# Kernel optimization log

Hardware: AMD Instinct MI355X
Metric: run time of the kernel (lower is better)

## Reference

```python
import jax, jax.numpy as jnp
import numpy as np

B, N, E = 2, 50000, 400000
C_IN, D, C, S, H, L, FFN = 5, 2, 128, 32, 8, 4, 512
COORD_F, TIME_F, FREQ_BASE, BETA = 8, 4, 1000.0, 1.0
HD = C // H


def setup_inputs() -> dict:
    key = jax.random.key(0)
    ks = jax.random.split(key, 32)
    sc = 0.02
    inp = {
        'inputs': jax.random.normal(ks[0], (B, N, C_IN), jnp.float32),
        'coords': jax.random.uniform(ks[1], (B, N, D), jnp.float32),
        't_norm': jax.random.uniform(ks[2], (B,), jnp.float32),
        'adj_indices': jax.random.randint(ks[3], (2, E), 0, N, jnp.int64 if jax.config.jax_enable_x64 else jnp.int32),
        'adj_values': jax.random.uniform(ks[4], (E,), jnp.float32) * 0.25,  # ~1/avg_degree for stable magnitudes
        'freq_matrix': jax.random.normal(ks[5], (D, COORD_F), jnp.float32),
        'embed_W': jax.random.normal(ks[6], (C_IN + 2 * COORD_F + 2 * TIME_F, C), jnp.float32) * sc,
        'embed_b': jnp.zeros((C,), jnp.float32),
        'ln1_g': jnp.ones((L, C), jnp.float32),
        'ln1_b': jnp.zeros((L, C), jnp.float32),
        'Wslice': jax.random.normal(ks[7], (L, C, S), jnp.float32) * sc,
        'bslice': jnp.zeros((L, S), jnp.float32),
        'Wfront': jax.random.normal(ks[8], (L, C, S), jnp.float32) * sc,
        'bfront': jnp.zeros((L, S), jnp.float32),
        'Win': jax.random.normal(ks[9], (L, C, 3 * C), jnp.float32) * sc,
        'b_in': jnp.zeros((L, 3 * C), jnp.float32),
        'Wout': jax.random.normal(ks[10], (L, C, C), jnp.float32) * sc,
        'bout': jnp.zeros((L, C), jnp.float32),
        'ln2_g': jnp.ones((L, C), jnp.float32),
        'ln2_b': jnp.zeros((L, C), jnp.float32),
        'Wff1': jax.random.normal(ks[11], (L, C, FFN), jnp.float32) * sc,
        'bff1': jnp.zeros((L, FFN), jnp.float32),
        'Wff2': jax.random.normal(ks[12], (L, FFN, C), jnp.float32) * sc,
        'bff2': jnp.zeros((L, C), jnp.float32),
        'proj_W': jax.random.normal(ks[13], (C, C_IN), jnp.float32) * sc,
        'proj_b': jnp.zeros((C_IN,), jnp.float32),
    }
    return inp


def _layer_norm(x, g, b, eps=1e-5):
    m = jnp.mean(x, -1, keepdims=True)
    v = jnp.mean(jnp.square(x - m), -1, keepdims=True)
    return (x - m) * jax.lax.rsqrt(v + eps) * g + b


def _forward(inputs, coords, t_norm, adj_indices, adj_values, freq_matrix,
             embed_W, embed_b, ln1_g, ln1_b, Wslice, bslice, Wfront, bfront,
             Win, b_in, Wout, bout, ln2_g, ln2_b, Wff1, bff1, Wff2, bff2,
             proj_W, proj_b):
    rows, cols = adj_indices[0], adj_indices[1]
    b, n = coords.shape[0], coords.shape[1]
    # spatial Fourier encoding (B,N,2*COORD_F)
    p = 2.0 * jnp.pi * (coords @ freq_matrix)
    sp_enc = jnp.concatenate([jnp.sin(p), jnp.cos(p)], -1)
    # temporal encoding (B,N,2*TIME_F)
    omega = FREQ_BASE ** (-jnp.arange(TIME_F, dtype=jnp.float32) / TIME_F)
    ang = omega[None, :] * (t_norm * FREQ_BASE)[:, None]
    t_enc = jnp.broadcast_to(jnp.concatenate([jnp.sin(ang), jnp.cos(ang)], -1)[:, None, :], (b, n, 2 * TIME_F))
    x = jnp.concatenate([inputs, sp_enc, t_enc], -1) @ embed_W + embed_b  # (B,N,C)
    weights_all = []
    for l in range(L):
        h = _layer_norm(x, ln1_g[l], ln1_b[l])
        # sparse adjacency aggregation: y[r] += a_e * h[c] (duplicates sum == coalesce)
        contrib = adj_values[None, :, None] * h[:, cols, :]  # (B,E,C)
        h_local = jax.vmap(lambda cb: jax.ops.segment_sum(cb, rows, num_segments=n))(contrib)
        h_front = h - h_local
        logits = h @ Wslice[l] + bslice[l] + BETA * (h_front @ Wfront[l] + bfront[l])
        w = jax.nn.softmax(logits, -1)  # (B,N,S)
        wsum = jnp.maximum(jnp.sum(w, axis=1)[:, :, None], 1e-8)  # (B,S,1)
        slices = jnp.einsum('bns,bnc->bsc', w, h) / wsum  # (B,S,C)
        # slice-space MHA (self-attention on S tokens)
        qkv = slices @ Win[l] + b_in[l]
        q, k, v = jnp.split(qkv, 3, axis=-1)
        def split_heads(t):
            return t.reshape(b, S, H, HD).transpose(0, 2, 1, 3)  # (B,H,S,HD)
        qh, kh, vh = split_heads(q), split_heads(k), split_heads(v)
        attn = jax.nn.softmax(jnp.einsum('bhqd,bhkd->bhqk', qh, kh) / jnp.sqrt(jnp.float32(HD)), -1)
        o = jnp.einsum('bhqk,bhkd->bhqd', attn, vh).transpose(0, 2, 1, 3).reshape(b, S, C)
        slices_out = o @ Wout[l] + bout[l]
        x = x + jnp.einsum('bns,bsc->bnc', w, slices_out)
        h2 = _layer_norm(x, ln2_g[l], ln2_b[l])
        x = x + jax.nn.gelu(h2 @ Wff1[l] + bff1[l], approximate=False) @ Wff2[l] + bff2[l]
        weights_all.append(w)
    out = x @ proj_W + proj_b  # (B,N,C_OUT)
    return out, jnp.stack(weights_all)  # (L,B,N,S)


def reference(inputs, coords, t_norm, adj_indices, adj_values, freq_matrix,
              embed_W, embed_b, ln1_g, ln1_b, Wslice, bslice, Wfront, bfront,
              Win, b_in, Wout, bout, ln2_g, ln2_b, Wff1, bff1, Wff2, bff2,
              proj_W, proj_b):
    return _forward(inputs, coords, t_norm, adj_indices, adj_values, freq_matrix,
                    embed_W, embed_b, ln1_g, ln1_b, Wslice, bslice, Wfront, bfront,
                    Win, b_in, Wout, bout, ln2_g, ln2_b, Wff1, bff1, Wff2, bff2,
                    proj_W, proj_b)
```

## Files before the change

kernel.cpp:

```cpp
#include <hip/hip_runtime.h>
#include <math.h>

#define BATCH 2
#define NN 50000
#define NE 400000
#define C_IN 5
#define CC 128
#define SS 32
#define NH 8
#define NL 4
#define FFN 512
#define COORD_F 8
#define TIME_F 4
#define HD 16
#define BETA 1.0f
#define TWO_PI 6.283185307179586476925287f

#define NTOT (BATCH * NN)
#define FF_MT 128
#define FF_BLOCKS ((NTOT + FF_MT - 1) / FF_MT)
#define MPAD (FF_BLOCKS * FF_MT)
#define NBLK ((NN + 127) / 128)
#define LP_PAD 136
#define H2S 136
#define HIDS 72
#define NREP 16
#define EMB_NPB 8
#define PROJ_NPB 12

typedef unsigned short u16;
typedef unsigned int u32;
typedef __attribute__((ext_vector_type(8))) __bf16 bf16x8;
typedef __attribute__((ext_vector_type(4))) float f32x4;

__device__ __forceinline__ u16 f2bf(float f) {
    union { __bf16 b; u16 u; } v;
    v.b = (__bf16)f;
    return v.u;
}

__device__ __forceinline__ float bf2f(u16 h) {
    union { u32 u; float f; } v; v.u = ((u32)h) << 16;
    return v.f;
}

__device__ __forceinline__ float bf_lo(u32 u) {
    union { u32 u; float f; } v; v.u = u << 16;
    return v.f;
}

__device__ __forceinline__ float bf_hi(u32 u) {
    union { u32 u; float f; } v; v.u = u & 0xffff0000u;
    return v.f;
}

__device__ __forceinline__ float gelu_f(float a) {
    float xx = a * 0.7071067811865475f;
    float ax = fabsf(xx);
    float t = 1.0f / fmaf(0.3275911f, ax, 1.0f);
    float poly = t * fmaf(t, fmaf(t, fmaf(t, fmaf(t, 1.061405429f, -1.453152027f),
                                          1.421413741f), -0.284496736f), 0.254829592f);
    float e = __expf(-ax * ax);
    float erfv = copysignf(fmaf(-poly, e, 1.0f), xx);
    return 0.5f * a * (1.0f + erfv);
}

__global__ void count_deg(const int* rows, int* deg) {
    int e = blockIdx.x * blockDim.x + threadIdx.x;
    if (e < NE) atomicAdd(&deg[rows[e]], 1);
}

__global__ __launch_bounds__(512) void scan_deg(const int* deg, int* rowptr) {
    __shared__ int part[512];
    int t = threadIdx.x;
    const int CH = (NN + 511) / 512;
    int begin = t * CH, end = min(begin + CH, NN);
    int s = 0;
    for (int i = begin; i < end; i++) s += deg[i];
    part[t] = s;
    __syncthreads();
    for (int off = 1; off < 512; off <<= 1) {
        int v = (t >= off) ? part[t - off] : 0;
        __syncthreads();
        part[t] += v;
        __syncthreads();
    }
    int base = (t == 0) ? 0 : part[t - 1];
    for (int i = begin; i < end; i++) { rowptr[i] = base; base += deg[i]; }
    if (t == 511) rowptr[NN] = part[511];
}

__global__ void fill_csr(const int* rows, const int* cols, const float* vals,
                         int* cursor, int* csr_col, float* csr_val) {
    int e = blockIdx.x * blockDim.x + threadIdx.x;
    if (e < NE) {
        int p = atomicAdd(&cursor[rows[e]], 1);
        csr_col[p] = cols[e];
        csr_val[p] = vals[e];
    }
}

__global__ __launch_bounds__(128) void embed_ln1_kernel(const float* __restrict__ inputs,
                                                        const float* __restrict__ coords,
                                                        const float* __restrict__ t_norm,
                                                        const float* __restrict__ freq,
                                                        const float* __restrict__ W,
                                                        const float* __restrict__ bias,
                                                        const float* __restrict__ g,
                                                        const float* __restrict__ bb,
                                                        float* __restrict__ x,
                                                        u16* __restrict__ hbf) {
    int t = threadIdx.x;
    int n0 = blockIdx.x * EMB_NPB;
    __shared__ float feat[EMB_NPB][32];
    __shared__ float sm[EMB_NPB][4];
    if (t < EMB_NPB) {
        int node = n0 + t;
        if (node < NTOT) {
            int b = node / NN;
            float c0 = coords[node * 2 + 0], c1 = coords[node * 2 + 1];
            #pragma unroll
            for (int j = 0; j < 8; j++) {
                float p = TWO_PI * (c0 * freq[j] + c1 * freq[8 + j]);
                feat[t][5 + j] = sinf(p);
                feat[t][13 + j] = cosf(p);
            }
            #pragma unroll
            for (int j = 0; j < 4; j++) {
                float omega = powf(1000.0f, -(float)j * 0.25f);
                float ang = omega * t_norm[b] * 1000.0f;
                feat[t][21 + j] = sinf(ang);
                feat[t][25 + j] = cosf(ang);
            }
            #pragma unroll
            for (int k = 0; k < 5; k++) feat[t][k] = inputs[node * 5 + k];
        }
    }
    float Wr[29];
    #pragma unroll
    for (int k = 0; k < 29; k++) Wr[k] = W[k * CC + t];
    float bi = bias[t], gt = g[t], bbt = bb[t];
    __syncthreads();
    float accv[EMB_NPB];
    #pragma unroll
    for (int nn = 0; nn < EMB_NPB; nn++) {
        float a = bi;
        #pragma unroll
        for (int k = 0; k < 29; k++) a += feat[nn][k] * Wr[k];
        accv[nn] = a;
        int node = n0 + nn;
        if (node < NTOT) x[(size_t)node * CC + t] = a;
    }
    #pragma unroll
    for (int nn = 0; nn < EMB_NPB; nn++) {
        float s = accv[nn];
        #pragma unroll
        for (int off = 32; off > 0; off >>= 1) s += __shfl_xor(s, off, 64);
        if ((t & 63) == 0) sm[nn][t >> 6] = s;
    }
    __syncthreads();
    float dv[EMB_NPB];
    #pragma unroll
    for (int nn = 0; nn < EMB_NPB; nn++) {
        float mean = (sm[nn][0] + sm[nn][1]) * (1.0f / 128.0f);
        float d = accv[nn] - mean;
        dv[nn] = d;
        float ss = d * d;
        #pragma unroll
        for (int off = 32; off > 0; off >>= 1) ss += __shfl_xor(ss, off, 64);
        if ((t & 63) == 0) sm[nn][2 + (t >> 6)] = ss;
    }
    __syncthreads();
    #pragma unroll
    for (int nn = 0; nn < EMB_NPB; nn++) {
        int node = n0 + nn;
        if (node < NTOT) {
            float var = (sm[nn][2] + sm[nn][3]) * (1.0f / 128.0f);
            hbf[(size_t)node * CC + t] = f2bf(dv[nn] * rsqrtf(var + 1e-5f) * gt + bbt);
        }
    }
}

__global__ __launch_bounds__(256) void agg_kernel(const u16* __restrict__ hbf,
                                                  const int* __restrict__ rowptr,
                                                  const int* __restrict__ csr_col,
                                                  const float* __restrict__ csr_val,
                                                  u16* __restrict__ hlbf) {
    int wid = threadIdx.x >> 6;
    int lane = threadIdx.x & 63;
    int node = blockIdx.x * 4 + wid;
    int b = node / NN, r = node - b * NN;
    int s0 = rowptr[r], s1 = rowptr[r + 1];
    const u32* hb = (const u32*)(hbf + (size_t)b * NN * CC);
    float a0l = 0.f, a1l = 0.f, a2l = 0.f, a3l = 0.f;
    float a0h = 0.f, a1h = 0.f, a2h = 0.f, a3h = 0.f;
    int e = s0;
    for (; e + 8 <= s1; e += 8) {
        int c0 = csr_col[e],     c1 = csr_col[e + 1], c2 = csr_col[e + 2], c3 = csr_col[e + 3];
        int c4 = csr_col[e + 4], c5 = csr_col[e + 5], c6 = csr_col[e + 6], c7 = csr_col[e + 7];
        float v0 = csr_val[e],     v1 = csr_val[e + 1], v2 = csr_val[e + 2], v3 = csr_val[e + 3];
        float v4 = csr_val[e + 4], v5 = csr_val[e + 5], v6 = csr_val[e + 6], v7 = csr_val[e + 7];
        u32 u0 = hb[(size_t)c0 * 64 + lane];
        u32 u1 = hb[(size_t)c1 * 64 + lane];
        u32 u2 = hb[(size_t)c2 * 64 + lane];
        u32 u3 = hb[(size_t)c3 * 64 + lane];
        u32 u4 = hb[(size_t)c4 * 64 + lane];
        u32 u5 = hb[(size_t)c5 * 64 + lane];
        u32 u6 = hb[(size_t)c6 * 64 + lane];
        u32 u7 = hb[(size_t)c7 * 64 + lane];
        a0l += v0 * bf_lo(u0);  a0h += v0 * bf_hi(u0);
        a1l += v1 * bf_lo(u1);  a1h += v1 * bf_hi(u1);
        a2l += v2 * bf_lo(u2);  a2h += v2 * bf_hi(u2);
        a3l += v3 * bf_lo(u3);  a3h += v3 * bf_hi(u3);
        a0l += v4 * bf_lo(u4);  a0h += v4 * bf_hi(u4);
        a1l += v5 * bf_lo(u5);  a1h += v5 * bf_hi(u5);
        a2l += v6 * bf_lo(u6);  a2h += v6 * bf_hi(u6);
        a3l += v7 * bf_lo(u7);  a3h += v7 * bf_hi(u7);
    }
    for (; e + 4 <= s1; e += 4) {
        int c0 = csr_col[e], c1 = csr_col[e + 1], c2 = csr_col[e + 2], c3 = csr_col[e + 3];
        float v0 = csr_val[e], v1 = csr_val[e + 1], v2 = csr_val[e + 2], v3 = csr_val[e + 3];
        u32 u0 = hb[(size_t)c0 * 64 + lane];
        u32 u1 = hb[(size_t)c1 * 64 + lane];
        u32 u2 = hb[(size_t)c2 * 64 + lane];
        u32 u3 = hb[(size_t)c3 * 64 + lane];
        a0l += v0 * bf_lo(u0);  a0h += v0 * bf_hi(u0);
        a1l += v1 * bf_lo(u1);  a1h += v1 * bf_hi(u1);
        a2l += v2 * bf_lo(u2);  a2h += v2 * bf_hi(u2);
        a3l += v3 * bf_lo(u3);  a3h += v3 * bf_hi(u3);
    }
    for (; e < s1; e++) {
        float v = csr_val[e];
        u32 u = hb[(size_t)csr_col[e] * 64 + lane];
        a0l += v * bf_lo(u);  a0h += v * bf_hi(u);
    }
    float al = (a0l + a1l) + (a2l + a3l);
    float ah = (a0h + a1h) + (a2h + a3h);
    u32 outv = (u32)f2bf(al) | ((u32)f2bf(ah) << 16);
    ((u32*)hlbf)[(size_t)node * 64 + lane] = outv;
}

__global__ __launch_bounds__(256) void pack_logits_weights(const float* Ws, const float* bs,
                                                           const float* Wf, const float* bf,
                                                           u16* Wcombp, float* bcombp) {
    int idx = blockIdx.x * 256 + threadIdx.x;
    if (idx >= NL * SS * 256) return;
    int l = idx / (SS * 256);
    int r = idx - l * (SS * 256);
    int s = r >> 8, k = r & 255;
    float v;
    if (k < 128)
        v = Ws[(size_t)l * CC * SS + (size_t)k * SS + s] + BETA * Wf[(size_t)l * CC * SS + (size_t)k * SS + s];
    else
        v = -BETA * Wf[(size_t)l * CC * SS + (size_t)(k - 128) * SS + s];
    Wcombp[idx] = f2bf(v);
    if (k == 0) bcombp[l * SS + s] = bs[l * SS + s] + BETA * bf[l * SS + s];
}

__global__ __launch_bounds__(256, 2) void logits_pool(const u16* __restrict__ hbf,
                                                      const u16* __restrict__ hlbf,
                                                      const u16* __restrict__ Wcomb,
                                                      const float* __restrict__ bcomb,
                                                      float* __restrict__ wout,
                                                      float* __restrict__ rep,
                                                      float* __restrict__ wsum) {
    __shared__ __align__(16) u16 hT[128 * LP_PAD];
    __shared__ __align__(16) u16 wTh[SS * LP_PAD];
    __shared__ __align__(16) u16 wTl[SS * LP_PAD];
    __shared__ float wsum_sh[SS];
    int t = threadIdx.x;
    int b = blockIdx.y;
    int nl0 = blockIdx.x * 128;
    int wv = t >> 6, lane = t & 63;
    int q = lane >> 4, ln16 = lane & 15;
    int nl0w = nl0 + wv * 32;
    if (t < SS) wsum_sh[t] = 0.0f;
    __syncthreads();

    f32x4 acc[2][2];
    #pragma unroll
    for (int mi = 0; mi < 2; mi++)
        #pragma unroll
        for (int ni = 0; ni < 2; ni++) acc[mi][ni] = (f32x4){0.f, 0.f, 0.f, 0.f};

    #pragma unroll
    for (int ks = 0; ks < 8; ks++) {
        const u16* src = (ks < 4) ? hbf : hlbf;
        int ko = (ks & 3) * 32 + q * 8;
        bf16x8 af[2], bfrg[2];
        #pragma unroll
        for (int mi = 0; mi < 2; mi++) {
            int nl = nl0w + mi * 16 + ln16;
            af[mi] = *(const bf16x8*)&src[((size_t)b * NN + nl) * CC + ko];
            if (ks < 4) {
                bool valid = nl < NN;
                const u16* ap = (const u16*)&af[mi];
                int nlb = nl - nl0;
                #pragma unroll
                for (int i = 0; i < 8; i++)
                    hT[(ko + i) * LP_PAD + nlb] = valid ? ap[i] : (u16)0;
            }
        }
        #pragma unroll
        for (int ni = 0; ni < 2; ni++)
            bfrg[ni] = *(const bf16x8*)&Wcomb[(size_t)(ni * 16 + ln16) * 256 + ks * 32 + q * 8];
        #pragma unroll
        for (int mi = 0; mi < 2; mi++)
            #pragma unroll
            for (int ni = 0; ni < 2; ni++)
                acc[mi][ni] = __builtin_amdgcn_mfma_f32_16x16x32_bf16(af[mi], bfrg[ni], acc[mi][ni], 0, 0, 0);
    }

    float bc0 = bcomb[ln16], bc1 = bcomb[16 + ln16];
    float ws0 = 0.0f, ws1 = 0.0f;
    #pragma unroll
    for (int mi = 0; mi < 2; mi++)
        #pragma unroll
        for (int r = 0; r < 4; r++) {
            float l0 = acc[mi][0][r] + bc0;
            float l1 = acc[mi][1][r] + bc1;
            float m = fmaxf(l0, l1);
            #pragma unroll
            for (int msk = 1; msk < 16; msk <<= 1) m = fmaxf(m, __shfl_xor(m, msk, 64));
            float e0 = __expf(l0 - m), e1 = __expf(l1 - m);
            float sum = e0 + e1;
            #pragma unroll
            for (int msk = 1; msk < 16; msk <<= 1) sum += __shfl_xor(sum, msk, 64);
            float is = 1.0f / sum;
            int nl = nl0w + mi * 16 + q * 4 + r;
            bool valid = nl < NN;
            float w0 = valid ? e0 * is : 0.0f;
            float w1 = valid ? e1 * is : 0.0f;
            u16 h0 = f2bf(w0), h1 = f2bf(w1);
            u16 lo0 = f2bf(w0 - bf2f(h0)), lo1 = f2bf(w1 - bf2f(h1));
            if (valid) {
                size_t gb = ((size_t)b * NN + nl) * SS;
                wout[gb + ln16] = w0;
                wout[gb + 16 + ln16] = w1;
            }
            int nlb = nl - nl0;
            wTh[ln16 * LP_PAD + nlb] = h0;  wTl[ln16 * LP_PAD + nlb] = lo0;
            wTh[(16 + ln16) * LP_PAD + nlb] = h1;  wTl[(16 + ln16) * LP_PAD + nlb] = lo1;
            ws0 += w0;  ws1 += w1;
        }
    ws0 += __shfl_xor(ws0, 16, 64); ws0 += __shfl_xor(ws0, 32, 64);
    ws1 += __shfl_xor(ws1, 16, 64); ws1 += __shfl_xor(ws1, 32, 64);
    if (q == 0) {
        atomicAdd(&wsum_sh[ln16], ws0);
        atomicAdd(&wsum_sh[16 + ln16], ws1);
    }
    __syncthreads();

    f32x4 pacc[2][8];
    #pragma unroll
    for (int st = 0; st < 2; st++)
        #pragma unroll
        for (int ct = 0; ct < 8; ct++) pacc[st][ct] = (f32x4){0.f, 0.f, 0.f, 0.f};
    {
        int kb = wv * 32 + q * 8;
        bf16x8 wh[2], wl2[2];
        #pragma unroll
        for (int st = 0; st < 2; st++) {
            wh[st] = *(const bf16x8*)&wTh[(st * 16 + ln16) * LP_PAD + kb];
            wl2[st] = *(const bf16x8*)&wTl[(st * 16 + ln16) * LP_PAD + kb];
        }
        #pragma unroll
        for (int ct = 0; ct < 8; ct++) {
            bf16x8 bfr = *(const bf16x8*)&hT[(ct * 16 + ln16) * LP_PAD + kb];
            #pragma unroll
            for (int st = 0; st < 2; st++) {
                pacc[st][ct] = __builtin_amdgcn_mfma_f32_16x16x32_bf16(wh[st], bfr, pacc[st][ct], 0, 0, 0);
                pacc[st][ct] = __builtin_amdgcn_mfma_f32_16x16x32_bf16(wl2[st], bfr, pacc[st][ct], 0, 0, 0);
            }
        }
    }
    __syncthreads();

    float* red = (float*)hT;
    for (int i = t; i < SS * CC; i += 256) red[i] = 0.0f;
    __syncthreads();
    #pragma unroll
    for (int st = 0; st < 2; st++)
        #pragma unroll
        for (int ct = 0; ct < 8; ct++)
            #pragma unroll
            for (int r = 0; r < 4; r++)
                atomicAdd(&red[(st * 16 + q * 4 + r) * CC + ct * 16 + ln16], pacc[st][ct][r]);
    __syncthreads();
    if (t < SS) atomicAdd(&wsum[b * SS + t], wsum_sh[t]);
    int rep_id = (blockIdx.y * NBLK + blockIdx.x) & (NREP - 1);
    float* dst = rep + ((size_t)rep_id * BATCH + b) * SS * CC;
    #pragma unroll
    for (int k = 0; k < 16; k++) {
        int idx = k * 256 + t;
        atomicAdd(&dst[idx], red[idx]);
    }
}

__global__ __launch_bounds__(128) void qkv_kernel(const float* __restrict__ rep,
                                                  const float* wsum,
                                                  const float* Win, const float* b_in_p,
                                                  float* qkv) {
    int blk = blockIdx.x;
    int b = blk >> 5;
    int t = threadIdx.x;
    __shared__ float row[128];
    int e = (blk & 31) * CC + t;
    float s = 0.0f;
    #pragma unroll
    for (int r = 0; r < NREP; r++) s += rep[((size_t)r * BATCH + b) * SS * CC + e];
    float iv = 1.0f / fmaxf(wsum[blk], 1e-8f);
    row[t] = s * iv;
    __syncthreads();
    #pragma unroll
    for (int jj = 0; jj < 3; jj++) {
        int j = t + jj * 128;
        float a = b_in_p[j];
        #pragma unroll 8
        for (int c = 0; c < 128; c++) a += row[c] * Win[c * 384 + j];
        qkv[(size_t)blk * 384 + j] = a;
    }
}

__global__ __launch_bounds__(64) void attn_kernel(const float* qkv, float* ovals) {
    int blk = blockIdx.x;
    int b = blk >> 3, h = blk & 7;
    int t = threadIdx.x;
    __shared__ float ksh[32 * 16], vsh[32 * 16];
    for (int i = t; i < 512; i += 64) {
        int k = i >> 4, d = i & 15;
        ksh[i] = qkv[((size_t)b * 32 + k) * 384 + 128 + h * 16 + d];
        vsh[i] = qkv[((size_t)b * 32 + k) * 384 + 256 + h * 16 + d];
    }
    __syncthreads();
    if (t < 32) {
        float qr[16];
        #pragma unroll
        for (int d = 0; d < 16; d++) qr[d] = qkv[((size_t)b * 32 + t) * 384 + h * 16 + d];
        float sc[32];
        float m = -1e30f;
        for (int k = 0; k < 32; k++) {
            float a = 0.0f;
            #pragma unroll
            for (int d = 0; d < 16; d++) a += qr[d] * ksh[k * 16 + d];
            a *= 0.25f;
            sc[k] = a;
            m = fmaxf(m, a);
        }
        float ssum = 0.0f;
        for (int k = 0; k < 32; k++) { float e = expf(sc[k] - m); sc[k] = e; ssum += e; }
        float is = 1.0f / ssum;
        float o[16];
        #pragma unroll
        for (int d = 0; d < 16; d++) o[d] = 0.0f;
        for (int k = 0; k < 32; k++) {
            float p = sc[k] * is;
            #pragma unroll
            for (int d = 0; d < 16; d++) o[d] += p * vsh[k * 16 + d];
        }
        #pragma unroll
        for (int d = 0; d < 16; d++) ovals[((size_t)b * 32 + t) * 128 + h * 16 + d] = o[d];
    }
}

__global__ __launch_bounds__(128) void mha_out_kernel(const float* ovals, const float* Wout,
                                                      const float* bout,
                                                      u16* soThi, u16* soTlo) {
    int blk = blockIdx.x;
    int b = blk >> 5, s = blk & 31;
    int t = threadIdx.x;
    __shared__ float row[128];
    row[t] = ovals[(size_t)blk * 128 + t];
    __syncthreads();
    float a = bout[t];
    #pragma unroll 8
    for (int cc = 0; cc < 128; cc++) a += row[cc] * Wout[cc * CC + t];
    u16 hi = f2bf(a);
    size_t idx = (size_t)b * CC * SS + (size_t)t * SS + s;
    soThi[idx] = hi;
    soTlo[idx] = f2bf(a - bf2f(hi));
}

__global__ __launch_bounds__(256) void pack_ffn_weights(const float* Wff1, const float* Wff2,
                                                        u16* W1p, u16* W2p) {
    int idx = blockIdx.x * 256 + threadIdx.x;
    if (idx >= NL * FFN * CC) return;
    int l = idx / (FFN * CC);
    int r = idx - l * (FFN * CC);
    int j = r >> 7, c = r & 127;
    W1p[idx] = f2bf(Wff1[(size_t)l * CC * FFN + (size_t)c * FFN + j]);
    int c2 = r >> 9, j2 = r & 511;
    W2p[idx] = f2bf(Wff2[(size_t)l * FFN * CC + (size_t)j2 * CC + c2]);
}

__global__ __launch_bounds__(256, 2) void ffn_mega(float* __restrict__ x,
                                                   const float* __restrict__ wfull,
                                                   const u16* __restrict__ soThi,
                                                   const u16* __restrict__ soTlo,
                                                   const float* __restrict__ g,
                                                   const float* __restrict__ bb,
                                                   const u16* __restrict__ W1p,
                                                   const float* __restrict__ bff1,
                                                   const u16* __restrict__ W2p,
                                                   const float* __restrict__ bff2,
                                                   const float* __restrict__ g1,
                                                   const float* __restrict__ b1,
                                                   u16* __restrict__ hbf_out) {
    __shared__ __align__(16) u16 smem[128 * 144];
    __shared__ __align__(16) float rowst[128 * 4];
    u16* h2t = smem;
    int t = threadIdx.x;
    int b = blockIdx.y;
    int n0 = blockIdx.x * 128;
    int wave = t >> 6, lane = t & 63;
    int wm = wave >> 1, wn = wave & 1;
    int q = lane >> 4, ln16 = lane & 15;
    bool emit = (g1 != nullptr);

    float gr[4], br[4];
    #pragma unroll
    for (int ni = 0; ni < 4; ni++) {
        int col = wn * 64 + ni * 16 + ln16;
        gr[ni] = g[col]; br[ni] = bb[col];
    }

    f32x4 acc2[4][4];
    #pragma unroll
    for (int mi = 0; mi < 4; mi++)
        #pragma unroll
        for (int ni = 0; ni < 4; ni++) acc2[mi][ni] = (f32x4){0.f, 0.f, 0.f, 0.f};

    {
        const u16* soh = soThi + (size_t)b * CC * SS;
        const u16* sol = soTlo + (size_t)b * CC * SS;
        bf16x8 bh[4], bl[4], ah[4], al[4];
        bf16x8 zf;
        #pragma unroll
        for (int i = 0; i < 8; i++) zf[i] = (__bf16)0.0f;
        #pragma unroll
        for (int ni = 0; ni < 4; ni++) {
            int c = wn * 64 + ni * 16 + ln16;
            bh[ni] = *(const bf16x8*)&soh[c * SS + q * 8];
            bl[ni] = *(const bf16x8*)&sol[c * SS + q * 8];
        }
        #pragma unroll
        for (int mi = 0; mi < 4; mi++) {
            int row = n0 + wm * 64 + mi * 16 + ln16;
            if (row < NN) {
                const float* wp = &wfull[((size_t)b * NN + row) * SS + q * 8];
                f32x4 wv0 = *(const f32x4*)wp;
                f32x4 wv1 = *(const f32x4*)(wp + 4);
                union { bf16x8 v; u16 u[8]; } uh, ul;
                #pragma unroll
                for (int i = 0; i < 4; i++) {
                    u16 h = f2bf(wv0[i]);
                    uh.u[i] = h;  ul.u[i] = f2bf(wv0[i] - bf2f(h));
                }
                #pragma unroll
                for (int i = 0; i < 4; i++) {
                    u16 h = f2bf(wv1[i]);
                    uh.u[4 + i] = h;  ul.u[4 + i] = f2bf(wv1[i] - bf2f(h));
                }
                ah[mi] = uh.v;  al[mi] = ul.v;
            } else { ah[mi] = zf; al[mi] = zf; }
        }
        #pragma unroll
        for (int mi = 0; mi < 4; mi++)
            #pragma unroll
            for (int ni = 0; ni < 4; ni++) {
                acc2[mi][ni] = __builtin_amdgcn_mfma_f32_16x16x32_bf16(ah[mi], bh[ni], acc2[mi][ni], 0, 0, 0);
                acc2[mi][ni] = __builtin_amdgcn_mfma_f32_16x16x32_bf16(al[mi], bh[ni], acc2[mi][ni], 0, 0, 0);
                acc2[mi][ni] = __builtin_amdgcn_mfma_f32_16x16x32_bf16(ah[mi], bl[ni], acc2[mi][ni], 0, 0, 0);
            }
    }

    #pragma unroll
    for (int mi = 0; mi < 4; mi++)
        #pragma unroll
        for (int r = 0; r < 4; r++) {
            int row = n0 + wm * 64 + mi * 16 + q * 4 + r;
            if (row < NN) {
                const float* xr = &x[((size_t)b * NN + row) * CC + wn * 64 + ln16];
                #pragma unroll
                for (int ni = 0; ni < 4; ni++) acc2[mi][ni][r] += xr[ni * 16];
            }
        }
    #pragma unroll
    for (int mi = 0; mi < 4; mi++)
        #pragma unroll
        for (int r = 0; r < 4; r++) {
            float a = acc2[mi][0][r] + acc2[mi][1][r] + acc2[mi][2][r] + acc2[mi][3][r];
            float a2 = acc2[mi][0][r] * acc2[mi][0][r] + acc2[mi][1][r] * acc2[mi][1][r] +
                       acc2[mi][2][r] * acc2[mi][2][r] + acc2[mi][3][r] * acc2[mi][3][r];
            #pragma unroll
            for (int msk = 1; msk < 16; msk <<= 1) {
                a += __shfl_xor(a, msk, 64);
                a2 += __shfl_xor(a2, msk, 64);
            }
            if (ln16 == 0) {
                int m = wm * 64 + mi * 16 + q * 4 + r;
                rowst[m * 4 + wn * 2] = a;
                rowst[m * 4 + wn * 2 + 1] = a2;
            }
        }
    __syncthreads();
    #pragma unroll
    for (int mi = 0; mi < 4; mi++)
        #pragma unroll
        for (int r = 0; r < 4; r++) {
            int m = wm * 64 + mi * 16 + q * 4 + r;
            float s1 = rowst[m * 4 + 0] + rowst[m * 4 + 2];
            float s2 = rowst[m * 4 + 1] + rowst[m * 4 + 3];
            float mean = s1 * (1.0f / 128.0f);
            float var = s2 * (1.0f / 128.0f) - mean * mean;
            float rstd = rsqrtf(fmaxf(var, 0.0f) + 1e-5f);
            #pragma unroll
            for (int ni = 0; ni < 4; ni++) {
                int col = wn * 64 + ni * 16 + ln16;
                h2t[m * H2S + col] = f2bf((acc2[mi][ni][r] - mean) * rstd * gr[ni] + br[ni]);
            }
        }
    __syncthreads();

    bf16x8 areg[4][4];
    #pragma unroll
    for (int ks = 0; ks < 4; ks++)
        #pragma unroll
        for (int mi = 0; mi < 4; mi++)
            areg[ks][mi] = *(const bf16x8*)&h2t[(wm * 64 + mi * 16 + ln16) * H2S + ks * 32 + q * 8];
    __syncthreads();

    for (int jc = 0; jc < 8; jc++) {
        u16* hid = smem + (jc & 1) * (128 * HIDS);
        f32x4 acc1[4][2];
        #pragma unroll
        for (int mi = 0; mi < 4; mi++)
            #pragma unroll
            for (int ni = 0; ni < 2; ni++) acc1[mi][ni] = (f32x4){0.f, 0.f, 0.f, 0.f};

        __builtin_amdgcn_s_setprio(1);
        #pragma unroll
        for (int ks = 0; ks < 4; ks++) {
            bf16x8 bfr[2];
            #pragma unroll
            for (int ni = 0; ni < 2; ni++)
                bfr[ni] = *(const bf16x8*)&W1p[(size_t)(jc * 64 + wn * 32 + ni * 16 + ln16) * CC + ks * 32 + q * 8];
            #pragma unroll
            for (int mi = 0; mi < 4; mi++)
                #pragma unroll
                for (int ni = 0; ni < 2; ni++)
                    acc1[mi][ni] = __builtin_amdgcn_mfma_f32_16x16x32_bf16(areg[ks][mi], bfr[ni], acc1[mi][ni], 0, 0, 0);
        }
        __builtin_amdgcn_s_setprio(0);

        #pragma unroll
        for (int ni = 0; ni < 2; ni++) {
            float b1v = bff1[jc * 64 + wn * 32 + ni * 16 + ln16];
            #pragma unroll
            for (int mi = 0; mi < 4; mi++)
                #pragma unroll
                for (int r = 0; r < 4; r++)
                    hid[(wm * 64 + mi * 16 + q * 4 + r) * HIDS + wn * 32 + ni * 16 + ln16] =
                        f2bf(gelu_f(acc1[mi][ni][r] + b1v));
        }
        __syncthreads();

        __builtin_amdgcn_s_setprio(1);
        #pragma unroll
        for (int ks2 = 0; ks2 < 2; ks2++) {
            bf16x8 af[4], bfr[4];
            #pragma unroll
            for (int mi = 0; mi < 4; mi++)
                af[mi] = *(const bf16x8*)&hid[(wm * 64 + mi * 16 + ln16) * HIDS + ks2 * 32 + q * 8];
            #pragma unroll
            for (int ni = 0; ni < 4; ni++)
                bfr[ni] = *(const bf16x8*)&W2p[(size_t)(wn * 64 + ni * 16 + ln16) * FFN + jc * 64 + ks2 * 32 + q * 8];
            #pragma unroll
            for (int mi = 0; mi < 4; mi++)
                #pragma unroll
                for (int ni = 0; ni < 4; ni++)
                    acc2[mi][ni] = __builtin_amdgcn_mfma_f32_16x16x32_bf16(af[mi], bfr[ni], acc2[mi][ni], 0, 0, 0);
        }
        __builtin_amdgcn_s_setprio(0);
    }

    float b2[4];
    #pragma unroll
    for (int ni = 0; ni < 4; ni++) b2[ni] = bff2[wn * 64 + ni * 16 + ln16];
    #pragma unroll
    for (int mi = 0; mi < 4; mi++)
        #pragma unroll
        for (int ni = 0; ni < 4; ni++)
            #pragma unroll
            for (int r = 0; r < 4; r++) acc2[mi][ni][r] += b2[ni];

    #pragma unroll
    for (int mi = 0; mi < 4; mi++)
        #pragma unroll
        for (int r = 0; r < 4; r++) {
            int row = n0 + wm * 64 + mi * 16 + q * 4 + r;
            if (row < NN) {
                float* xo = &x[((size_t)b * NN + row) * CC + wn * 64 + ln16];
                #pragma unroll
                for (int ni = 0; ni < 4; ni++) xo[ni * 16] = acc2[mi][ni][r];
            }
        }

    if (emit) {
        float g1r[4], b1r[4];
        #pragma unroll
        for (int ni = 0; ni < 4; ni++) {
            int col = wn * 64 + ni * 16 + ln16;
            g1r[ni] = g1[col]; b1r[ni] = b1[col];
        }
        #pragma unroll
        for (int mi = 0; mi < 4; mi++)
            #pragma unroll
            for (int r = 0; r < 4; r++) {
                float a = acc2[mi][0][r] + acc2[mi][1][r] + acc2[mi][2][r] + acc2[mi][3][r];
                float a2 = acc2[mi][0][r] * acc2[mi][0][r] + acc2[mi][1][r] * acc2[mi][1][r] +
                           acc2[mi][2][r] * acc2[mi][2][r] + acc2[mi][3][r] * acc2[mi][3][r];
                #pragma unroll
                for (int msk = 1; msk < 16; msk <<= 1) {
                    a += __shfl_xor(a, msk, 64);
                    a2 += __shfl_xor(a2, msk, 64);
                }
                if (ln16 == 0) {
                    int m = wm * 64 + mi * 16 + q * 4 + r;
                    rowst[m * 4 + wn * 2] = a;
                    rowst[m * 4 + wn * 2 + 1] = a2;
                }
            }
        __syncthreads();
        #pragma unroll
        for (int mi = 0; mi < 4; mi++)
            #pragma unroll
            for (int r = 0; r < 4; r++) {
                int m = wm * 64 + mi * 16 + q * 4 + r;
                float s1 = rowst[m * 4 + 0] + rowst[m * 4 + 2];
                float s2 = rowst[m * 4 + 1] + rowst[m * 4 + 3];
                float mean = s1 * (1.0f / 128.0f);
                float var = s2 * (1.0f / 128.0f) - mean * mean;
                float rstd = rsqrtf(fmaxf(var, 0.0f) + 1e-5f);
                #pragma unroll
                for (int ni = 0; ni < 4; ni++) {
                    int col = wn * 64 + ni * 16 + ln16;
                    smem[m * H2S + col] = f2bf((acc2[mi][ni][r] - mean) * rstd * g1r[ni] + b1r[ni]);
                }
            }
        __syncthreads();
        #pragma unroll
        for (int it = 0; it < 8; it++) {
            int chunk = it * 256 + t;
            int m = chunk >> 4;
            int c8 = (chunk & 15) << 3;
            int row = n0 + m;
            if (row < NN)
                *(f32x4*)&hbf_out[((size_t)b * NN + row) * CC + c8] =
                    *(const f32x4*)&smem[m * H2S + c8];
        }
    }
}

__global__ __launch_bounds__(128) void proj_kernel(const float* __restrict__ x,
                                                   const float* __restrict__ W,
                                                   const float* __restrict__ bias,
                                                   float* __restrict__ outp) {
    int t = threadIdx.x;
    int n0 = blockIdx.x * PROJ_NPB;
    __shared__ float xr[PROJ_NPB][128];
    __shared__ float pr[3][40];
    for (int idx = t; idx < PROJ_NPB * 128; idx += 128) {
        int nn = idx >> 7, c = idx & 127;
        int node = n0 + nn;
        xr[nn][c] = (node < NTOT) ? x[(size_t)node * CC + c] : 0.0f;
    }
    __syncthreads();
    for (int pass = 0; pass < 4; pass++) {
        if (t < 120) {
            int nl = t / 40, tt = t - nl * 40;
            int k = tt / 8, part = tt % 8;
            float a = 0.0f;
            #pragma unroll
            for (int i = 0; i < 16; i++) {
                int c = part * 16 + i;
                a += xr[pass * 3 + nl][c] * W[c * C_IN + k];
            }
            pr[nl][tt] = a;
        }
        __syncthreads();
        if (t < 15) {
            int nl = t / 5, k = t - nl * 5;
            int node = n0 + pass * 3 + nl;
            if (node < NTOT) {
                float a = bias[k];
                #pragma unroll
                for (int p = 0; p < 8; p++) a += pr[nl][k * 8 + p];
                outp[(size_t)node * C_IN + k] = a;
            }
        }
        __syncthreads();
    }
}

extern "C" void kernel_launch(void* const* d_in, const int* in_sizes, int n_in,
                              void* d_out, int out_size, void* d_ws, size_t ws_size,
                              hipStream_t stream) {
    const float* inputs  = (const float*)d_in[0];
    const float* coords  = (const float*)d_in[1];
    const float* t_norm  = (const float*)d_in[2];
    const int*   adj     = (const int*)d_in[3];
    const float* adj_v   = (const float*)d_in[4];
    const float* freq    = (const float*)d_in[5];
    const float* embed_W = (const float*)d_in[6];
    const float* embed_b = (const float*)d_in[7];
    const float* ln1_g   = (const float*)d_in[8];
    const float* ln1_b   = (const float*)d_in[9];
    const float* Wslice  = (const float*)d_in[10];
    const float* bslice  = (const float*)d_in[11];
    const float* Wfront  = (const float*)d_in[12];
    const float* bfront  = (const float*)d_in[13];
    const float* Win     = (const float*)d_in[14];
    const float* b_in    = (const float*)d_in[15];
    const float* Wout    = (const float*)d_in[16];
    const float* bout    = (const float*)d_in[17];
    const float* ln2_g   = (const float*)d_in[18];
    const float* ln2_b   = (const float*)d_in[19];
    const float* Wff1    = (const float*)d_in[20];
    const float* bff1    = (const float*)d_in[21];
    const float* Wff2    = (const float*)d_in[22];
    const float* bff2    = (const float*)d_in[23];
    const float* proj_W  = (const float*)d_in[24];
    const float* proj_b  = (const float*)d_in[25];

    float* out = (float*)d_out;
    float* wout_base = out + (size_t)BATCH * NN * C_IN;

    float* x          = (float*)d_ws;
    u16*   hbf        = (u16*)(x + (size_t)NTOT * CC);
    u16*   hlbf       = hbf + (size_t)MPAD * CC;
    u16*   soThi      = hlbf + (size_t)MPAD * CC;
    u16*   soTlo      = soThi + BATCH * CC * SS;
    float* qkv_ws     = (float*)(soTlo + BATCH * CC * SS);
    float* ovals_ws   = qkv_ws + BATCH * SS * 384;
    float* csr_val    = ovals_ws + BATCH * SS * CC;
    int*   rowptr     = (int*)(csr_val + NE);
    int*   cursor     = rowptr + (NN + 1);
    int*   deg        = cursor + NN;
    int*   csr_col    = deg + NN;
    u16*   W1p        = (u16*)(csr_col + NE);
    u16*   W2p        = W1p + NL * FFN * CC;
    u16*   Wcombp     = W2p + NL * CC * FFN;
    float* bcomb      = (float*)(Wcombp + NL * SS * 256);
    float* rep        = bcomb + NL * SS;
    float* wsum       = rep + (size_t)NREP * BATCH * SS * CC;

    hipMemsetAsync(deg, 0, NN * sizeof(int), stream);
    count_deg<<<(NE + 255) / 256, 256, 0, stream>>>(adj, deg);
    scan_deg<<<1, 512, 0, stream>>>(deg, rowptr);
    hipMemcpyAsync(cursor, rowptr, NN * sizeof(int), hipMemcpyDeviceToDevice, stream);
    fill_csr<<<(NE + 255) / 256, 256, 0, stream>>>(adj, adj + NE, adj_v, cursor, csr_col, csr_val);

    pack_ffn_weights<<<(NL * FFN * CC + 255) / 256, 256, 0, stream>>>(Wff1, Wff2, W1p, W2p);
    pack_logits_weights<<<(NL * SS * 256 + 255) / 256, 256, 0, stream>>>(Wslice, bslice, Wfront,
                                                                         bfront, Wcombp, bcomb);

    embed_ln1_kernel<<<(NTOT + EMB_NPB - 1) / EMB_NPB, 128, 0, stream>>>(
        inputs, coords, t_norm, freq, embed_W, embed_b, ln1_g, ln1_b, x, hbf);

    for (int l = 0; l < NL; l++) {
        float* wl = wout_base + (size_t)l * NTOT * SS;
        agg_kernel<<<NTOT / 4, 256, 0, stream>>>(hbf, rowptr, csr_col, csr_val, hlbf);
        hipMemsetAsync(rep, 0, ((size_t)NREP * BATCH * SS * CC + BATCH * SS) * sizeof(float), stream);
        dim3 glp(NBLK, BATCH);
        logits_pool<<<glp, 256, 0, stream>>>(hbf, hlbf, Wcombp + (size_t)l * SS * 256,
                                             bcomb + l * SS, wl, rep, wsum);
        qkv_kernel<<<BATCH * SS, 128, 0, stream>>>(rep, wsum,
                                                   Win + (size_t)l * CC * 3 * CC,
                                                   b_in + l * 3 * CC, qkv_ws);
        attn_kernel<<<BATCH * NH, 64, 0, stream>>>(qkv_ws, ovals_ws);
        mha_out_kernel<<<BATCH * SS, 128, 0, stream>>>(ovals_ws, Wout + (size_t)l * CC * CC,
                                                       bout + l * CC, soThi, soTlo);
        const float* g1n = (l + 1 < NL) ? (ln1_g + (size_t)(l + 1) * CC) : nullptr;
        const float* b1n = (l + 1 < NL) ? (ln1_b + (size_t)(l + 1) * CC) : nullptr;
        dim3 g3(NBLK, BATCH);
        ffn_mega<<<g3, 256, 0, stream>>>(x, wl, soThi, soTlo,
                                         ln2_g + l * CC, ln2_b + l * CC,
                                         W1p + (size_t)l * FFN * CC, bff1 + l * FFN,
                                         W2p + (size_t)l * CC * FFN, bff2 + l * CC,
                                         g1n, b1n, hbf);
    }

    proj_kernel<<<(NTOT + PROJ_NPB - 1) / PROJ_NPB, 128, 0, stream>>>(x, proj_W, proj_b, out);
}
```

Before: 1.717 ms.

## Split slice-aggregation MFMA by output columns per wave, drop LDS reduction

The slice-token aggregation GEMM previously split the K (node) dimension across the four waves, which meant a zero-fill, shared-memory atomic reduction and two extra barriers before the global atomics. Now each wave owns two 16-column output tiles and loops over the full K range, so its accumulators are complete and go straight to global atomicAdd. This removes the LDS reduction and its syncs but serialises the K loop within each wave and changes the layout of the global atomic stores.

```diff
diff --git a/kernel.cpp b/kernel.cpp
--- a/kernel.cpp
+++ b/kernel.cpp
@@ -351,50 +351,43 @@
     }
     __syncthreads();
 
-    f32x4 pacc[2][8];
+    f32x4 pacc[2][2];
     #pragma unroll
     for (int st = 0; st < 2; st++)
         #pragma unroll
-        for (int ct = 0; ct < 8; ct++) pacc[st][ct] = (f32x4){0.f, 0.f, 0.f, 0.f};
-    {
-        int kb = wv * 32 + q * 8;
-        bf16x8 wh[2], wl2[2];
+        for (int ctl = 0; ctl < 2; ctl++) pacc[st][ctl] = (f32x4){0.f, 0.f, 0.f, 0.f};
+    #pragma unroll
+    for (int ks = 0; ks < 4; ks++) {
+        int kb = ks * 32 + q * 8;
+        bf16x8 wh[2], wl2[2], bfr[2];
         #pragma unroll
         for (int st = 0; st < 2; st++) {
             wh[st] = *(const bf16x8*)&wTh[(st * 16 + ln16) * LP_PAD + kb];
             wl2[st] = *(const bf16x8*)&wTl[(st * 16 + ln16) * LP_PAD + kb];
         }
         #pragma unroll
-        for (int ct = 0; ct < 8; ct++) {
-            bf16x8 bfr = *(const bf16x8*)&hT[(ct * 16 + ln16) * LP_PAD + kb];
+        for (int ctl = 0; ctl < 2; ctl++)
+            bfr[ctl] = *(const bf16x8*)&hT[((wv * 2 + ctl) * 16 + ln16) * LP_PAD + kb];
+        #pragma unroll
+        for (int ctl = 0; ctl < 2; ctl++)
             #pragma unroll
             for (int st = 0; st < 2; st++) {
-                pacc[st][ct] = __builtin_amdgcn_mfma_f32_16x16x32_bf16(wh[st], bfr, pacc[st][ct], 0, 0, 0);
-                pacc[st][ct] = __builtin_amdgcn_mfma_f32_16x16x32_bf16(wl2[st], bfr, pacc[st][ct], 0, 0, 0);
-            }
-        }
-    }
-    __syncthreads();
-
-    float* red = (float*)hT;
-    for (int i = t; i < SS * CC; i += 256) red[i] = 0.0f;
-    __syncthreads();
-    #pragma unroll
-    for (int st = 0; st < 2; st++)
-        #pragma unroll
-        for (int ct = 0; ct < 8; ct++)
-            #pragma unroll
-            for (int r = 0; r < 4; r++)
-                atomicAdd(&red[(st * 16 + q * 4 + r) * CC + ct * 16 + ln16], pacc[st][ct][r]);
-    __syncthreads();
+                pacc[st][ctl] = __builtin_amdgcn_mfma_f32_16x16x32_bf16(wh[st], bfr[ctl], pacc[st][ctl], 0, 0, 0);
+                pacc[st][ctl] = __builtin_amdgcn_mfma_f32_16x16x32_bf16(wl2[st], bfr[ctl], pacc[st][ctl], 0, 0, 0);
+            }
+    }
+
     if (t < SS) atomicAdd(&wsum[b * SS + t], wsum_sh[t]);
     int rep_id = (blockIdx.y * NBLK + blockIdx.x) & (NREP - 1);
     float* dst = rep + ((size_t)rep_id * BATCH + b) * SS * CC;
     #pragma unroll
-    for (int k = 0; k < 16; k++) {
-        int idx = k * 256 + t;
-        atomicAdd(&dst[idx], red[idx]);
-    }
+    for (int st = 0; st < 2; st++)
+        #pragma unroll
+        for (int ctl = 0; ctl < 2; ctl++)
+            #pragma unroll
+            for (int r = 0; r < 4; r++)
+                atomicAdd(&dst[(st * 16 + q * 4 + r) * CC + (wv * 2 + ctl) * 16 + ln16],
+                          pacc[st][ctl][r]);
 }
 
 __global__ __launch_bounds__(128) void qkv_kernel(const float* __restrict__ rep,
```

Result: faster. 1.462 ms, median of 2 (-14.8%).
